# Performance work log

Hardware: AMD Instinct MI355X
Metric: run time of the kernel (lower is better)

Reference implementation:

```python
import jax, jax.numpy as jnp
import numpy as np

C = 684      # encoder out_channels
H = 256      # hidden_size
I = 256      # input_size (embedding dim)
A = 512      # attention dim
V = 415      # word_num (vocab)
CCOV = 256   # coverage conv channels
K = 11       # coverage conv kernel
HF, WF = 32, 128  # feature map H', W'
RATIO = 16
T = 64       # fixed number of decode steps


def gru_cell(x, h, Wih, Whh, bih, bhh):
    # torch.nn.GRUCell semantics
    gi = x @ Wih.T + bih
    gh = h @ Whh.T + bhh
    ir, iz, inn = jnp.split(gi, 3, axis=-1)
    hr, hz, hn = jnp.split(gh, 3, axis=-1)
    r = jax.nn.sigmoid(ir + hr)
    z = jax.nn.sigmoid(iz + hz)
    n = jnp.tanh(inn + r * hn)
    return (1.0 - z) * n + z * h


def setup_inputs() -> dict:
    key = jax.random.key(0)
    ks = list(jax.random.split(key, 40))
    s = 0.05
    def rn(shape):
        return jax.random.normal(ks.pop(), shape, dtype=jnp.float32) * s
    p = {}
    p['cnn_features'] = jax.random.normal(ks.pop(), (1, C, HF, WF), dtype=jnp.float32)
    p['images_mask'] = jnp.ones((1, 1, HF * RATIO, WF * RATIO), dtype=jnp.float32)
    p['emb_table'] = rn((V, I))
    p['W_init'] = rn((H, C)); p['b_init'] = jnp.zeros((H,), jnp.float32)
    p['Wih_in'] = rn((3 * H, I)); p['Whh_in'] = rn((3 * H, H))
    p['bih_in'] = jnp.zeros((3 * H,), jnp.float32); p['bhh_in'] = jnp.zeros((3 * H,), jnp.float32)
    p['Wih_out'] = rn((3 * H, C)); p['Whh_out'] = rn((3 * H, H))
    p['bih_out'] = jnp.zeros((3 * H,), jnp.float32); p['bhh_out'] = jnp.zeros((3 * H,), jnp.float32)
    p['Wq'] = rn((A, H)); p['bq'] = jnp.zeros((A,), jnp.float32)
    p['Wproj'] = rn((A, C)); p['bproj'] = jnp.zeros((A,), jnp.float32)
    p['conv_k'] = rn((CCOV, 1, K, K))
    p['Wcov'] = rn((A, CCOV))
    p['wa'] = rn((A,)); p['ba'] = jnp.zeros((), jnp.float32)
    p['Ws'] = rn((H // 2, H)); p['bs'] = jnp.zeros((H // 2,), jnp.float32)
    p['We'] = rn((H // 2, I)); p['be'] = jnp.zeros((H // 2,), jnp.float32)
    p['Wc'] = rn((H // 2, C)); p['bc'] = jnp.zeros((H // 2,), jnp.float32)
    p['Wv'] = rn((V, H // 2)); p['bv'] = jnp.zeros((V,), jnp.float32)
    return p


def _decode(cnn_features, images_mask, emb_table, W_init, b_init,
            Wih_in, Whh_in, bih_in, bhh_in, Wih_out, Whh_out, bih_out, bhh_out,
            Wq, bq, Wproj, bproj, conv_k, Wcov, wa, ba,
            Ws, bs, We, be, Wc, bc, Wv, bv):
    mask = images_mask[:, :, ::RATIO, ::RATIO]          # [1,1,HF,WF]
    avg = jnp.sum(cnn_features * mask, axis=(2, 3)) / jnp.sum(mask, axis=(2, 3))  # [1,C]
    h0 = jnp.tanh(avg @ W_init.T + b_init)               # init_hidden
    cnn_trans = jnp.einsum('bchw,ac->bhwa', cnn_features, Wproj) + bproj  # 1x1 proj, [1,HF,WF,A]
    mask2d = mask[:, 0] > 0                              # [1,HF,WF]
    emb0 = emb_table[jnp.ones((1,), dtype=jnp.int32)]    # embedding(torch.ones(1).long())
    alpha_sum0 = jnp.zeros((1, 1, HF, WF), dtype=cnn_features.dtype)

    def attend(hidden, alpha_sum):
        q = hidden @ Wq.T + bq                           # [1,A]
        cov = jax.lax.conv_general_dilated(alpha_sum, conv_k, (1, 1), [(K // 2, K // 2)] * 2)
        cov_t = jnp.einsum('bchw,ac->bhwa', cov, Wcov)   # [1,HF,WF,A]
        e = jnp.tanh(q[:, None, None, :] + cov_t + cnn_trans)
        energy = jnp.einsum('bhwa,a->bhw', e, wa) + ba
        energy = jnp.where(mask2d, energy, -1e9)
        alpha = jax.nn.softmax(energy.reshape(1, -1), axis=-1).reshape(energy.shape)
        alpha_sum = alpha_sum + alpha[:, None]
        ctx = jnp.einsum('bhw,bchw->bc', alpha, cnn_features)  # [1,C]
        return ctx, alpha_sum

    def step(carry, _):
        emb, h_par, a_sum = carry
        h1 = gru_cell(emb, h_par, Wih_in, Whh_in, bih_in, bhh_in)      # word_input_gru
        ctx, a_sum = attend(h1, a_sum)                                  # word_attention
        h = gru_cell(ctx, h1, Wih_out, Whh_out, bih_out, bhh_out)       # word_out_gru
        state = (h @ Ws.T + bs) + (emb @ We.T + be) + (ctx @ Wc.T + bc) # fused out state
        prob = state @ Wv.T + bv                                        # word_convert, [1,V]
        word = jnp.argmax(prob, axis=-1)                                # greedy feedback
        emb_next = emb_table[word]
        return (emb_next, h, a_sum), prob[0]

    _, probs = jax.lax.scan(step, (emb0, h0, alpha_sum0), None, length=T)
    return probs  # [T, V]


def reference(cnn_features, images_mask, emb_table, W_init, b_init,
              Wih_in, Whh_in, bih_in, bhh_in, Wih_out, Whh_out, bih_out, bhh_out,
              Wq, bq, Wproj, bproj, conv_k, Wcov, wa, ba,
              Ws, bs, We, be, Wc, bc, Wv, bv):
    return _decode(cnn_features, images_mask, emb_table, W_init, b_init,
                   Wih_in, Whh_in, bih_in, bhh_in, Wih_out, Whh_out, bih_out, bhh_out,
                   Wq, bq, Wproj, bproj, conv_k, Wcov, wa, ba,
                   Ws, bs, We, be, Wc, bc, Wv, bv)
```

## Files before the change

kernel.cpp:

```cpp
#include <hip/hip_runtime.h>
#include <math.h>

#define HF 32
#define WF 128
#define HW 4096
#define C_DIM 684
#define H_DIM 256
#define A_DIM 512
#define V_DIM 415
#define PADR 42
#define PADC 144
#define T_STEPS 64

#define NERG 128
#define CTX0 128
#define NCTXB 86
#define MONO 214
#define RED0 215
#define TAIL0 223
#define HEAT0 239
#define NGRID 255

constexpr int CT_OFF      = 0;
constexpr int KMT_OFF     = CT_OFF + HW * A_DIM;
constexpr int APAD_OFF    = KMT_OFF + 61952;
constexpr int MASK_OFF    = APAD_OFF + 6048;
constexpr int PART_OFF    = MASK_OFF + 4096;
constexpr int AVG_OFF     = PART_OFF + 16384;
constexpr int H0_OFF      = AVG_OFF + 704;
constexpr int QV_OFF      = H0_OFF + 256;
constexpr int H1V_OFF     = QV_OFF + 512;
constexpr int GHOV_OFF    = H1V_OFF + 512;
constexpr int GHNV_OFF    = GHOV_OFF + 1536;
constexpr int GS_OFF      = GHNV_OFF + 768;
constexpr int GPS_OFF     = GS_OFF + 6144;
constexpr int MSUM_OFF    = GPS_OFF + 1024;
constexpr int FLAGS_OFF   = MSUM_OFF + 16;
constexpr int AFR_OFF     = FLAGS_OFF + 4096;
constexpr int AF2R_OFF    = AFR_OFF + 128;
constexpr int H1F_OFF     = AF2R_OFF + 128;
constexpr int DONE_OFF    = H1F_OFF + 128;
constexpr int GFR_OFF     = DONE_OFF + 128;
constexpr int TQR_OFF     = GFR_OFF + 1024;
constexpr int SYNC_END    = TQR_OFF + 2048;
constexpr int PGIO2_OFF   = SYNC_END;
constexpr int PSC2_OFF    = PGIO2_OFF + NCTXB * 768;
constexpr int GI_OFF      = PSC2_OFF + NCTXB * 128;
constexpr int SE_OFF      = GI_OFF + V_DIM * 768;
constexpr int WIHTOUT_OFF = SE_OFF + V_DIM * 128;
constexpr int WCT_OFF     = WIHTOUT_OFF + 684 * 768;
constexpr int WST_OFF     = WCT_OFF + 684 * 128;
constexpr int WVT_OFF     = WST_OFF + 256 * 128;
constexpr int WS_END      = WVT_OFF + 128 * V_DIM;

__device__ __forceinline__ float sigmoidf_(float x) { return 1.f / (1.f + expf(-x)); }
__device__ __forceinline__ float ftanh(float x) {
  float e = __expf(2.f * x);
  return 1.f - 2.f / (e + 1.f);
}

__device__ __forceinline__ float gld(const float* p) {
  int v = __hip_atomic_load((const int*)p, __ATOMIC_RELAXED, __HIP_MEMORY_SCOPE_AGENT);
  return __int_as_float(v);
}
__device__ __forceinline__ void gst(float* p, float x) {
  __hip_atomic_store((int*)p, __float_as_int(x), __ATOMIC_RELAXED, __HIP_MEMORY_SCOPE_AGENT);
}
__device__ __forceinline__ void pollf(int* p, int ph) {
  int it = 0;
  while (__hip_atomic_load(p, __ATOMIC_RELAXED, __HIP_MEMORY_SCOPE_AGENT) < ph) {
    if (it < 4) __builtin_amdgcn_s_sleep(1);
    else if (it < 16) __builtin_amdgcn_s_sleep(4);
    else __builtin_amdgcn_s_sleep(8);
    ++it;
  }
  asm volatile("" ::: "memory");
}
__device__ __forceinline__ void rel_store(int* p, int v) {
  __hip_atomic_store(p, v, __ATOMIC_RELEASE, __HIP_MEMORY_SCOPE_AGENT);
}


__global__ void k_init(const float* __restrict__ imask, float* ws) {
  __shared__ float red[4];
  int tid = threadIdx.x;
  float s = 0.f;
  for (int i = tid; i < HW; i += 256) {
    int h = i >> 7, w = i & 127;
    float m = imask[h * 16 * 2048 + w * 16];
    ws[MASK_OFF + i] = m;
    s += m;
  }
  for (int i = tid; i < PADR * PADC; i += 256) ws[APAD_OFF + i] = 0.f;
  int* sync = (int*)(ws + FLAGS_OFF);
  for (int i = tid; i < 7680; i += 256) sync[i] = 0;
#pragma unroll
  for (int off = 32; off; off >>= 1) s += __shfl_xor(s, off, 64);
  if ((tid & 63) == 0) red[tid >> 6] = s;
  __syncthreads();
  if (tid == 0) ws[MSUM_OFF] = red[0] + red[1] + red[2] + red[3];
}

__global__ void k_avg(const float* __restrict__ cnn, float* ws) {
  __shared__ float red[4];
  int c = blockIdx.x, tid = threadIdx.x;
  const float* row = cnn + c * HW;
  float s = 0.f;
  for (int i = tid; i < HW; i += 256) s += ws[MASK_OFF + i] * row[i];
#pragma unroll
  for (int off = 32; off; off >>= 1) s += __shfl_xor(s, off, 64);
  if ((tid & 63) == 0) red[tid >> 6] = s;
  __syncthreads();
  if (tid == 0) ws[AVG_OFF + c] = (red[0] + red[1] + red[2] + red[3]) / ws[MSUM_OFF];
}

__global__ void k_h0(const float* __restrict__ W_init, const float* __restrict__ b_init, float* ws) {
  __shared__ float a_s[C_DIM];
  int tid = threadIdx.x;
  for (int i = tid; i < C_DIM; i += 256) a_s[i] = ws[AVG_OFF + i];
  __syncthreads();
  const float* wr = W_init + tid * C_DIM;
  float s = b_init[tid];
  for (int k = 0; k < C_DIM; k++) s += a_s[k] * wr[k];
  ws[H0_OFF + tid] = tanhf(s);
}

__global__ __launch_bounds__(512) void k_km(const float* __restrict__ convk,
                                            const float* __restrict__ Wcov, float* ws) {
  __shared__ float kt[256];
  int t = blockIdx.x, a = threadIdx.x;
  if (a < 256) kt[a] = convk[a * 121 + t];
  __syncthreads();
  const float* wr = Wcov + a * 256;
  float s = 0.f;
  for (int c = 0; c < 256; c++) s += kt[c] * wr[c];
  ws[KMT_OFF + a * 121 + t] = s;
}

__global__ void k_ct(const float* __restrict__ cnn, const float* __restrict__ Wproj,
                     const float* __restrict__ bproj, float* ws) {
  __shared__ float As[8][128];
  __shared__ float Bs[8][64];
  int hw0 = blockIdx.x * 128;
  int a0 = blockIdx.y * 64;
  int tid = threadIdx.x;
  int tx = tid & 15, ty = tid >> 4;
  float acc[8][4];
#pragma unroll
  for (int i = 0; i < 8; i++)
#pragma unroll
    for (int j = 0; j < 4; j++) acc[i][j] = 0.f;
  for (int c0 = 0; c0 < C_DIM; c0 += 8) {
    {
      int kk = tid >> 5;
      int m4 = (tid & 31) * 4;
      int c = c0 + kk;
      float4 v = make_float4(0.f, 0.f, 0.f, 0.f);
      if (c < C_DIM) v = *(const float4*)(cnn + c * HW + hw0 + m4);
      *(float4*)&As[kk][m4] = v;
    }
    {
      int n = tid & 63;
      int kk0 = (tid >> 6) * 2;
      const float* wr = Wproj + (a0 + n) * C_DIM + c0;
      Bs[kk0][n]     = (c0 + kk0 < C_DIM) ? wr[kk0] : 0.f;
      Bs[kk0 + 1][n] = (c0 + kk0 + 1 < C_DIM) ? wr[kk0 + 1] : 0.f;
    }
    __syncthreads();
#pragma unroll
    for (int kk = 0; kk < 8; kk++) {
      float a8[8], b4[4];
#pragma unroll
      for (int i = 0; i < 8; i++) a8[i] = As[kk][ty * 8 + i];
#pragma unroll
      for (int j = 0; j < 4; j++) b4[j] = Bs[kk][tx * 4 + j];
#pragma unroll
      for (int i = 0; i < 8; i++)
#pragma unroll
        for (int j = 0; j < 4; j++) acc[i][j] += a8[i] * b4[j];
    }
    __syncthreads();
  }
#pragma unroll
  for (int i = 0; i < 8; i++) {
    int hw = hw0 + ty * 8 + i;
#pragma unroll
    for (int j = 0; j < 4; j++) {
      int a = a0 + tx * 4 + j;
      ws[CT_OFF + hw * A_DIM + a] = acc[i][j] + bproj[a];
    }
  }
}

__global__ void k_gi(const float* __restrict__ emb_table, const float* __restrict__ Wih_in,
                     const float* __restrict__ bih_in, float* ws) {
  __shared__ float e_s[256];
  int v = blockIdx.x, tid = threadIdx.x;
  e_s[tid] = emb_table[v * 256 + tid];
  __syncthreads();
#pragma unroll
  for (int r = 0; r < 3; r++) {
    int m = r * 256 + tid;
    const float* wr = Wih_in + m * 256;
    float s = bih_in[m];
    for (int k = 0; k < 256; k++) s += e_s[k] * wr[k];
    ws[GI_OFF + v * 768 + m] = s;
  }
}

__global__ void k_se(const float* __restrict__ emb_table, const float* __restrict__ We,
                     const float* __restrict__ be, float* ws) {
  __shared__ float e_s[256];
  int v = blockIdx.x, tid = threadIdx.x;
  e_s[tid] = emb_table[v * 256 + tid];
  e_s[tid + 128] = emb_table[v * 256 + tid + 128];
  __syncthreads();
  const float* wr = We + tid * 256;
  float s = be[tid];
  for (int k = 0; k < 256; k++) s += e_s[k] * wr[k];
  ws[SE_OFF + v * 128 + tid] = s;
}

__global__ void k_tr(const float* __restrict__ in, float* __restrict__ out, int M, int Kd) {
  int total = M * Kd;
  for (int i = blockIdx.x * blockDim.x + threadIdx.x; i < total; i += gridDim.x * blockDim.x) {
    int m = i / Kd, k = i - m * Kd;
    out[k * M + m] = in[i];
  }
}

__global__ __launch_bounds__(512) void k_pre0(const float* __restrict__ Whh_in,
                                              const float* __restrict__ bhh_in, float* ws) {
  __shared__ float h0s[256];
  __shared__ float ghn48[48];
  const int s = blockIdx.x, tid = threadIdx.x;
  const int j0 = s * 16;
  if (tid < 256) h0s[tid] = ws[H0_OFF + tid];
  __syncthreads();
  {
    int r = tid >> 3, l = tid & 7;
    if (r < 48) {
      int mg = (r >> 4) * 256 + j0 + (r & 15);
      const float* wr = Whh_in + mg * 256 + l * 32;
      float sm = 0.f;
#pragma unroll
      for (int k = 0; k < 32; k++) sm += h0s[l * 32 + k] * wr[k];
#pragma unroll
      for (int off = 4; off; off >>= 1) sm += __shfl_xor(sm, off, 8);
      if (l == 0) ghn48[r] = sm + bhh_in[mg];
    }
  }
  __syncthreads();
  if (tid < 16) {
    int j = j0 + tid;
    const float* gi = ws + GI_OFF + 1 * 768;
    float r = sigmoidf_(gi[j] + ghn48[tid]);
    float z = sigmoidf_(gi[256 + j] + ghn48[16 + tid]);
    float n = tanhf(gi[512 + j] + r * ghn48[32 + tid]);
    gst(ws + H1V_OFF + j, (1.f - z) * n + z * h0s[j]);
  }
}

__global__ __launch_bounds__(512) void k_pre1(const float* __restrict__ Wq,
                                              const float* __restrict__ Whh_out,
                                              const float* __restrict__ bhh_out, float* ws) {
  __shared__ float h1s[256];
  const int s = blockIdx.x, tid = threadIdx.x;
  if (tid < 256) h1s[tid] = gld(ws + H1V_OFF + tid);
  __syncthreads();
  {
    int ap = tid >> 4, l = tid & 15;
    int a = s * 32 + ap;
    const float* wr = Wq + a * 256 + l * 16;
    float sm = 0.f;
#pragma unroll
    for (int k = 0; k < 16; k++) sm += h1s[l * 16 + k] * wr[k];
#pragma unroll
    for (int off = 8; off; off >>= 1) sm += __shfl_xor(sm, off, 16);
    if (l == 0) gst(ws + QV_OFF + a, sm);
  }
  {
    int r = tid >> 3, l = tid & 7;
    if (r < 48) {
      int m = s * 48 + r;
      const float* wr = Whh_out + m * 256 + l * 32;
      float sm = 0.f;
#pragma unroll
      for (int k = 0; k < 32; k++) sm += h1s[l * 32 + k] * wr[k];
#pragma unroll
      for (int off = 4; off; off >>= 1) sm += __shfl_xor(sm, off, 8);
      if (l == 0) gst(ws + GHOV_OFF + m, sm + bhh_out[m]);
    }
  }
}

__global__ void k_go(float* ws) {
  int tid = threadIdx.x;
  if (tid < 128) ((int*)(ws + TQR_OFF))[tid * 16] = 1;
}


__global__ __launch_bounds__(512) void k_steps(
    const float* __restrict__ cnn, const float* __restrict__ Whh_in,
    const float* __restrict__ Whh_out, const float* __restrict__ Wq,
    const float* __restrict__ bq, const float* __restrict__ wa, const float* __restrict__ ba,
    const float* __restrict__ bih_out, const float* __restrict__ bhh_out,
    const float* __restrict__ bhh_in,
    const float* __restrict__ bs_, const float* __restrict__ bc_, const float* __restrict__ bv_,
    float* ws, float* __restrict__ out) {
  __shared__ __align__(16) float S[40016];

  const int bid = blockIdx.x, tid = threadIdx.x;
  int* flags = (int*)(ws + FLAGS_OFF);
  int* afr   = (int*)(ws + AFR_OFF);
  int* af2r  = (int*)(ws + AF2R_OFF);
  int* h1f   = (int*)(ws + H1F_OFF);
  int* donef = (int*)(ws + DONE_OFF);
  int* gfr   = (int*)(ws + GFR_OFF);
  int* tqr   = (int*)(ws + TQR_OFF);

  if (bid < NERG) {
    const int h_row = bid >> 2, aq = bid & 3, a0 = aq * 128;
    const int al = tid & 127, hslot = tid >> 7;
    float* km    = S;
    float* ct    = S + 16896;
    float* patch = S + 33280;
    float* maskv = S + 34864;
    float* redE  = S + 34992;
    for (int i = tid; i < 128 * 132; i += 512) {
      int a = i / 132, j = i - a * 132;
      int dy = j / 12, dx = j - dy * 12;
      km[i] = (dx < 11) ? ws[KMT_OFF + (a0 + a) * 121 + dy * 11 + dx] : 0.f;
    }
    for (int i = tid; i < 128 * 128; i += 512) {
      int w = i >> 7, aa = i & 127;
      ct[i] = ws[CT_OFF + (h_row * 128 + w) * 512 + a0 + aa];
    }
    if (tid < 128) maskv[tid] = ws[MASK_OFF + h_row * 128 + tid];
    const float bq_a = bq[a0 + al], wa_a = wa[a0 + al], ba0 = ba[0];
    __syncthreads();

#pragma unroll 1
    for (int t = 0; t < T_STEPS; t++) {
      if (tid == 0) pollf(&af2r[(bid & 7) * 16], t);
      __syncthreads();
      for (int i = tid; i < 11 * 138; i += 512) {
        int r = i / 138, c = i - r * 138;
        patch[r * 144 + c] = gld(ws + APAD_OFF + (h_row + r) * PADC + c);
      }
      __syncthreads();
      float acc[2][16];
#pragma unroll
      for (int p = 0; p < 2; p++)
#pragma unroll
        for (int i = 0; i < 16; i++) acc[p][i] = 0.f;
      const int wbase0 = hslot * 32;
#pragma unroll 1
      for (int dy = 0; dy < 11; dy++) {
        float kv[12];
        {
          const float* kb = &km[al * 132 + dy * 12];
          *(float4*)&kv[0] = *(const float4*)&kb[0];
          *(float4*)&kv[4] = *(const float4*)&kb[4];
          *(float4*)&kv[8] = *(const float4*)&kb[8];
        }
#pragma unroll
        for (int p = 0; p < 2; p++) {
          float row[28];
          const float* pr = &patch[dy * 144 + wbase0 + p * 16];
#pragma unroll
          for (int i = 0; i < 7; i++) *(float4*)&row[i * 4] = *(const float4*)&pr[i * 4];
#pragma unroll
          for (int dx = 0; dx < 11; dx++)
#pragma unroll
            for (int wi = 0; wi < 16; wi++) acc[p][wi] += kv[dx] * row[wi + dx];
        }
      }
      if (tid < 16) pollf(&tqr[(tid * 8 + (bid & 7)) * 16], t + 1);
      __syncthreads();
      float qa = bq_a + gld(ws + QV_OFF + a0 + al);
#pragma unroll 1
      for (int p = 0; p < 2; p++) {
        const int wbase = wbase0 + p * 16;
#pragma unroll
        for (int wi = 0; wi < 16; wi++) {
          float x = acc[p][wi] + qa + ct[(wbase + wi) * 128 + al];
          float v = ftanh(x) * wa_a;
#pragma unroll
          for (int off = 32; off; off >>= 1) v += __shfl_xor(v, off, 64);
          if ((tid & 63) == 0) redE[(tid >> 6) * 16 + wi] = v;
        }
        __syncthreads();
        if (tid < 64) {
          int hs2 = tid >> 4, wi = tid & 15;
          int w = hs2 * 32 + p * 16 + wi;
          float e = redE[(hs2 * 2) * 16 + wi] + redE[(hs2 * 2 + 1) * 16 + wi];
          float val = (maskv[w] > 0.f) ? (e + (aq == 0 ? ba0 : 0.f)) : -2.5e8f;
          gst(ws + PART_OFF + aq * 4096 + h_row * 128 + w, val);
        }
        __syncthreads();
      }
      if (tid == 0) rel_store(&flags[bid * 16], t + 1);
    }

  } else if (bid < CTX0 + NCTXB) {
    const int cb = bid - CTX0, c0 = cb * 8;
    float* cnnS = S;
    float* wio  = S + 32768;
    float* wct  = S + 38912;
    float* redC = S + 39936;
    float* ctxv = S + 40000;
    float* invp = S + 40008;
    for (int i = tid; i < 8 * 4096; i += 512) {
      int c = c0 + (i >> 12);
      cnnS[i] = (c < C_DIM) ? cnn[c * 4096 + (i & 4095)] : 0.f;
    }
    for (int i = tid; i < 8 * 768; i += 512) {
      int c = c0 + i / 768;
      wio[i] = (c < C_DIM) ? ws[WIHTOUT_OFF + c * 768 + (i % 768)] : 0.f;
    }
    for (int i = tid; i < 8 * 128; i += 512) {
      int c = c0 + (i >> 7);
      wct[i] = (c < C_DIM) ? ws[WCT_OFF + c * 128 + (i & 127)] : 0.f;
    }
    __syncthreads();

#pragma unroll 1
    for (int t = 0; t < T_STEPS; t++) {
      if (tid == 0) pollf(&afr[(bid & 7) * 16], t + 1);
      __syncthreads();
      float ev[8];
      float ssum = 0.f;
#pragma unroll
      for (int j = 0; j < 8; j++) {
        int hw = j * 512 + tid;
        float e = gld(ws + PART_OFF + hw) + gld(ws + PART_OFF + 4096 + hw) +
                  gld(ws + PART_OFF + 8192 + hw) + gld(ws + PART_OFF + 12288 + hw);
        ev[j] = __expf(e);
        ssum += ev[j];
      }
#pragma unroll
      for (int off = 32; off; off >>= 1) ssum += __shfl_xor(ssum, off, 64);
      if ((tid & 63) == 0) redC[tid >> 6] = ssum;
      __syncthreads();
      if (tid == 0) {
        float s2 = 0.f;
#pragma unroll
        for (int i = 0; i < 8; i++) s2 += redC[i];
        invp[0] = 1.f / s2;
      }
      __syncthreads();
      float inv = invp[0];
      if (cb < 8) {
        int hw = cb * 512 + tid;
        int hh = hw >> 7, ww = hw & 127;
        float* ap = ws + APAD_OFF + (hh + 5) * PADC + ww + 5;
        gst(ap, gld(ap) + ev[cb] * inv);
      }
#pragma unroll
      for (int cc = 0; cc < 8; cc++) {
        float p = 0.f;
#pragma unroll
        for (int j = 0; j < 8; j++) p += ev[j] * cnnS[cc * 4096 + j * 512 + tid];
#pragma unroll
        for (int off = 32; off; off >>= 1) p += __shfl_xor(p, off, 64);
        if ((tid & 63) == 0) redC[(tid >> 6) * 8 + cc] = p;
      }
      __syncthreads();
      if (tid < 8) {
        float cv = 0.f;
#pragma unroll
        for (int w2 = 0; w2 < 8; w2++) cv += redC[w2 * 8 + tid];
        ctxv[tid] = cv * inv;
      }
      __syncthreads();
      for (int m = tid; m < 768; m += 512) {
        float s2 = 0.f;
#pragma unroll
        for (int cc = 0; cc < 8; cc++) s2 += ctxv[cc] * wio[cc * 768 + m];
        gst(ws + PGIO2_OFF + cb * 768 + m, s2);
      }
      if (tid < 128) {
        float s2 = 0.f;
#pragma unroll
        for (int cc = 0; cc < 8; cc++) s2 += ctxv[cc] * wct[cc * 128 + tid];
        gst(ws + PSC2_OFF + cb * 128 + tid, s2);
      }
      __syncthreads();
      if (tid == 0) rel_store(&flags[(CTX0 + cb) * 16], t + 1);
    }

  } else if (bid == MONO) {
    float* wst  = S;
    float* mh   = S + 32768;
    float* mst  = S + 33024;
    float* sval = S + 33152;
    int*   sidx = (int*)(S + 33664);
    int*   mwp  = (int*)(S + 34176);
    int*   mwn  = (int*)(S + 34177);
    for (int i = tid; i < 256 * 128; i += 512) wst[i] = ws[WST_OFF + i];
    if (tid == 0) mwp[0] = 1;
    __syncthreads();

#pragma unroll 1
    for (int t = 0; t < T_STEPS; t++) {
      const int par = t & 1;
      if (tid < 128) pollf(&flags[tid * 16], t + 1);
      __syncthreads();
      if (tid < 8) rel_store(&afr[tid * 16], t + 1);
      if (tid < 8) pollf(&gfr[(tid * 8 + 7) * 16], t + 1);
      __syncthreads();
      if (tid < 256) {
        float g0 = bih_out[tid], g1 = bih_out[256 + tid], g2 = bih_out[512 + tid];
#pragma unroll
        for (int j = 0; j < 8; j++) {
          const float* gs = ws + GS_OFF + j * 768;
          g0 += gld(gs + tid);
          g1 += gld(gs + 256 + tid);
          g2 += gld(gs + 512 + tid);
        }
        const float* gh = ws + GHOV_OFF + par * 768;
        float o0 = gld(gh + tid), o1 = gld(gh + 256 + tid), o2 = gld(gh + 512 + tid);
        float h1v = gld(ws + H1V_OFF + par * 256 + tid);
        float r = sigmoidf_(g0 + o0);
        float z = sigmoidf_(g1 + o1);
        float n = tanhf(g2 + r * o2);
        mh[tid] = (1.f - z) * n + z * h1v;
      }
      __syncthreads();
      if (tid < 128) {
        float s = bs_[tid] + bc_[tid] + ws[SE_OFF + mwp[0] * 128 + tid];
#pragma unroll
        for (int j = 0; j < 8; j++) s += gld(ws + GPS_OFF + j * 128 + tid);
        const float* wt = wst + tid;
#pragma unroll 8
        for (int k = 0; k < 256; k++) s += mh[k] * wt[k * 128];
        mst[tid] = s;
      }
      __syncthreads();
      {
        float best = -3.4e38f;
        if (tid < V_DIM) {
          float p2 = bv_[tid];
          const float* wt = ws + WVT_OFF + tid;
#pragma unroll 8
          for (int k = 0; k < 128; k++) p2 += mst[k] * wt[k * V_DIM];
          out[t * V_DIM + tid] = p2;
          best = p2;
        }
        sval[tid] = best;
        sidx[tid] = tid;
        __syncthreads();
        for (int m = 256; m >= 1; m >>= 1) {
          if (tid < m) {
            float ov = sval[tid + m];
            int oi = sidx[tid + m];
            if (ov > sval[tid] || (ov == sval[tid] && oi < sidx[tid])) {
              sval[tid] = ov;
              sidx[tid] = oi;
            }
          }
          __syncthreads();
        }
        if (tid == 0) mwn[0] = sidx[0];
        __syncthreads();
      }
      if (tid < 16) pollf(&flags[(224 + tid) * 16], t + 1);
      __syncthreads();
      if (tid < 256) {
        const float* gi = ws + GI_OFF + mwn[0] * 768;
        float n0 = gld(ws + GHNV_OFF + tid);
        float n1 = gld(ws + GHNV_OFF + 256 + tid);
        float n2 = gld(ws + GHNV_OFF + 512 + tid);
        float r = sigmoidf_(gi[tid] + n0);
        float z = sigmoidf_(gi[256 + tid] + n1);
        float n = tanhf(gi[512 + tid] + r * n2);
        gst(ws + H1V_OFF + ((t + 1) & 1) * 256 + tid, (1.f - z) * n + z * mh[tid]);
      }
      __syncthreads();
      if (tid < 8) rel_store(&h1f[tid * 16], t + 1);
      if (tid == 0) mwp[0] = mwn[0];
      __syncthreads();
    }
    if (tid < 8) rel_store(&donef[tid * 16], 1);

  } else if (bid < TAIL0) {
    const int j = bid - RED0;
    const int lo = j * 11, hi = (j == 7) ? 86 : (lo + 11);
#pragma unroll 1
    for (int t = 0; t < T_STEPS; t++) {
      if (tid < hi - lo) pollf(&flags[(CTX0 + lo + tid) * 16], t + 1);
      __syncthreads();
      if (j == 0 && tid < 8) rel_store(&af2r[tid * 16], t + 1);
      for (int m = tid; m < 768; m += 512) {
        float s = 0.f;
        for (int cb = lo; cb < hi; cb++) s += gld(ws + PGIO2_OFF + cb * 768 + m);
        gst(ws + GS_OFF + j * 768 + m, s);
      }
      if (tid < 128) {
        float s = 0.f;
        for (int cb = lo; cb < hi; cb++) s += gld(ws + PSC2_OFF + cb * 128 + tid);
        gst(ws + GPS_OFF + j * 128 + tid, s);
      }
      __syncthreads();
      if (tid < 8) rel_store(&gfr[(j * 8 + tid) * 16], t + 1);
    }

  } else if (bid < HEAT0) {
    const int s = bid - TAIL0;
    float* whinS = S;
    float* whoS  = S + 12288;
    float* wqS   = S + 24576;
    float* hS    = S + 32768;
    float* h1S   = S + 33024;
    for (int i = tid; i < 12288; i += 512) whinS[i] = Whh_in[s * 12288 + i];
    for (int i = tid; i < 12288; i += 512) whoS[i] = Whh_out[s * 12288 + i];
    for (int i = tid; i < 8192; i += 512) wqS[i] = Wq[s * 8192 + i];
    __syncthreads();

#pragma unroll 1
    for (int t = 0; t < T_STEPS; t++) {
      const int par = t & 1;
      if (tid < 8) pollf(&gfr[(tid * 8 + (s & 7)) * 16], t + 1);
      __syncthreads();
      if (tid < 256) {
        float g0 = bih_out[tid], g1 = bih_out[256 + tid], g2 = bih_out[512 + tid];
#pragma unroll
        for (int j = 0; j < 8; j++) {
          const float* gs = ws + GS_OFF + j * 768;
          g0 += gld(gs + tid);
          g1 += gld(gs + 256 + tid);
          g2 += gld(gs + 512 + tid);
        }
        const float* gh = ws + GHOV_OFF + par * 768;
        float o0 = gld(gh + tid), o1 = gld(gh + 256 + tid), o2 = gld(gh + 512 + tid);
        float h1v = gld(ws + H1V_OFF + par * 256 + tid);
        float r = sigmoidf_(g0 + o0);
        float z = sigmoidf_(g1 + o1);
        float n = tanhf(g2 + r * o2);
        hS[tid] = (1.f - z) * n + z * h1v;
      }
      __syncthreads();
      {
        int r = tid >> 3, l = tid & 7;
        if (r < 48) {
          int m = s * 48 + r;
          const float* wr = &whinS[r * 256 + l * 32];
          const float* hb = &hS[l * 32];
          float sm = 0.f;
#pragma unroll
          for (int k = 0; k < 32; k += 4) {
            float4 w4 = *(const float4*)&wr[k];
            float4 h4 = *(const float4*)&hb[k];
            sm += w4.x * h4.x + w4.y * h4.y + w4.z * h4.z + w4.w * h4.w;
          }
#pragma unroll
          for (int off = 4; off; off >>= 1) sm += __shfl_xor(sm, off, 8);
          if (l == 0) gst(ws + GHNV_OFF + m, sm + bhh_in[m]);
        }
      }
      __syncthreads();
      if (tid == 0) rel_store(&flags[(224 + s) * 16], t + 1);
      if (tid == 0) pollf(&h1f[(s & 7) * 16], t + 1);
      __syncthreads();
      if (tid < 256) h1S[tid] = gld(ws + H1V_OFF + ((t + 1) & 1) * 256 + tid);
      __syncthreads();
      {
        int r = tid >> 3, l = tid & 7;
        if (r < 48) {
          int m = s * 48 + r;
          const float* wr = &whoS[r * 256 + l * 32];
          const float* hb = &h1S[l * 32];
          float sm = 0.f;
#pragma unroll
          for (int k = 0; k < 32; k += 4) {
            float4 w4 = *(const float4*)&wr[k];
            float4 h4 = *(const float4*)&hb[k];
            sm += w4.x * h4.x + w4.y * h4.y + w4.z * h4.z + w4.w * h4.w;
          }
#pragma unroll
          for (int off = 4; off; off >>= 1) sm += __shfl_xor(sm, off, 8);
          if (l == 0) gst(ws + GHOV_OFF + ((t + 1) & 1) * 768 + m, sm + bhh_out[m]);
        }
      }
      {
        int ap = tid >> 4, l = tid & 15;
        int a = s * 32 + ap;
        const float* wr = &wqS[ap * 256 + l * 16];
        const float* hb = &h1S[l * 16];
        float sm = 0.f;
#pragma unroll
        for (int k = 0; k < 16; k++) sm += wr[k] * hb[k];
#pragma unroll
        for (int off = 8; off; off >>= 1) sm += __shfl_xor(sm, off, 16);
        if (l == 0) gst(ws + QV_OFF + a, sm);
      }
      __syncthreads();
      if (tid < 8) rel_store(&tqr[(s * 8 + tid) * 16], t + 2);
    }

  } else {
    volatile int* hstop = (volatile int*)(S + 100);
    if (tid == 0) *hstop = 0;
    __syncthreads();
    if (tid < 256) {
      float a0 = 1.f + (float)tid, a1 = 2.f, a2 = 3.f, a3 = 4.f;
      const float b = 0.9999f, c = 1e-7f;
      while (*hstop == 0) {
#pragma unroll
        for (int i = 0; i < 16; i++) {
          a0 = __builtin_fmaf(a0, b, c);
          a1 = __builtin_fmaf(a1, b, c);
          a2 = __builtin_fmaf(a2, b, c);
          a3 = __builtin_fmaf(a3, b, c);
        }
        if (tid == 0 &&
            __hip_atomic_load(&donef[(bid & 7) * 16], __ATOMIC_RELAXED,
                              __HIP_MEMORY_SCOPE_AGENT) != 0)
          *hstop = 1;
      }
      asm volatile("" :: "v"(a0), "v"(a1), "v"(a2), "v"(a3));
    }
  }
}


extern "C" void kernel_launch(void* const* d_in, const int* in_sizes, int n_in,
                              void* d_out, int out_size, void* d_ws, size_t ws_size,
                              hipStream_t stream) {
  (void)in_sizes; (void)n_in; (void)out_size; (void)ws_size;
  const float* cnn      = (const float*)d_in[0];
  const float* imask    = (const float*)d_in[1];
  const float* emb_tab  = (const float*)d_in[2];
  const float* W_init   = (const float*)d_in[3];
  const float* b_init   = (const float*)d_in[4];
  const float* Wih_in   = (const float*)d_in[5];
  const float* Whh_in   = (const float*)d_in[6];
  const float* bih_in   = (const float*)d_in[7];
  const float* bhh_in   = (const float*)d_in[8];
  const float* Wih_out  = (const float*)d_in[9];
  const float* Whh_out  = (const float*)d_in[10];
  const float* bih_out  = (const float*)d_in[11];
  const float* bhh_out  = (const float*)d_in[12];
  const float* Wq       = (const float*)d_in[13];
  const float* bq       = (const float*)d_in[14];
  const float* Wproj    = (const float*)d_in[15];
  const float* bproj    = (const float*)d_in[16];
  const float* convk    = (const float*)d_in[17];
  const float* Wcov     = (const float*)d_in[18];
  const float* wa       = (const float*)d_in[19];
  const float* ba       = (const float*)d_in[20];
  const float* Ws_      = (const float*)d_in[21];
  const float* bs_      = (const float*)d_in[22];
  const float* We_      = (const float*)d_in[23];
  const float* be_      = (const float*)d_in[24];
  const float* Wc_      = (const float*)d_in[25];
  const float* bc_      = (const float*)d_in[26];
  const float* Wv_      = (const float*)d_in[27];
  const float* bv_      = (const float*)d_in[28];
  float* ws  = (float*)d_ws;
  float* out = (float*)d_out;

  k_init<<<1, 256, 0, stream>>>(imask, ws);
  k_avg<<<C_DIM, 256, 0, stream>>>(cnn, ws);
  k_h0<<<1, 256, 0, stream>>>(W_init, b_init, ws);
  k_km<<<121, 512, 0, stream>>>(convk, Wcov, ws);
  k_ct<<<dim3(HW / 128, A_DIM / 64), 256, 0, stream>>>(cnn, Wproj, bproj, ws);
  k_gi<<<V_DIM, 256, 0, stream>>>(emb_tab, Wih_in, bih_in, ws);
  k_se<<<V_DIM, 128, 0, stream>>>(emb_tab, We_, be_, ws);
  k_tr<<<512, 256, 0, stream>>>(Wih_out, ws + WIHTOUT_OFF, 768, 684);
  k_tr<<<512, 256, 0, stream>>>(Wc_, ws + WCT_OFF, 128, 684);
  k_tr<<<512, 256, 0, stream>>>(Ws_, ws + WST_OFF, 128, 256);
  k_tr<<<512, 256, 0, stream>>>(Wv_, ws + WVT_OFF, 415, 128);
  k_pre0<<<16, 512, 0, stream>>>(Whh_in, bhh_in, ws);
  k_pre1<<<16, 512, 0, stream>>>(Wq, Whh_out, bhh_out, ws);
  k_go<<<1, 256, 0, stream>>>(ws);

  k_steps<<<NGRID, 512, 0, stream>>>(cnn, Whh_in, Whh_out, Wq, bq, wa, ba,
                                     bih_out, bhh_out, bhh_in, bs_, bc_, bv_, ws, out);
}
```

Baseline: 2.980 ms.

## Move context projection into reducer blocks and pad LDS weight rows

```diff
diff --git a/kernel.cpp b/kernel.cpp
--- a/kernel.cpp
+++ b/kernel.cpp
@@ -34,7 +34,8 @@
 constexpr int GHNV_OFF    = GHOV_OFF + 1536;
 constexpr int GS_OFF      = GHNV_OFF + 768;
 constexpr int GPS_OFF     = GS_OFF + 6144;
-constexpr int MSUM_OFF    = GPS_OFF + 1024;
+constexpr int CTXV_OFF    = GPS_OFF + 1024;
+constexpr int MSUM_OFF    = CTXV_OFF + 704;
 constexpr int FLAGS_OFF   = MSUM_OFF + 16;
 constexpr int AFR_OFF     = FLAGS_OFF + 4096;
 constexpr int AF2R_OFF    = AFR_OFF + 128;
@@ -43,9 +44,7 @@
 constexpr int GFR_OFF     = DONE_OFF + 128;
 constexpr int TQR_OFF     = GFR_OFF + 1024;
 constexpr int SYNC_END    = TQR_OFF + 2048;
-constexpr int PGIO2_OFF   = SYNC_END;
-constexpr int PSC2_OFF    = PGIO2_OFF + NCTXB * 768;
-constexpr int GI_OFF      = PSC2_OFF + NCTXB * 128;
+constexpr int GI_OFF      = SYNC_END;
 constexpr int SE_OFF      = GI_OFF + V_DIM * 768;
 constexpr int WIHTOUT_OFF = SE_OFF + V_DIM * 128;
 constexpr int WCT_OFF     = WIHTOUT_OFF + 684 * 768;
@@ -406,22 +405,12 @@
   } else if (bid < CTX0 + NCTXB) {
     const int cb = bid - CTX0, c0 = cb * 8;
     float* cnnS = S;
-    float* wio  = S + 32768;
-    float* wct  = S + 38912;
-    float* redC = S + 39936;
-    float* ctxv = S + 40000;
-    float* invp = S + 40008;
+    float* redC = S + 32768;
+    float* ctxv = S + 32832;
+    float* invp = S + 32840;
     for (int i = tid; i < 8 * 4096; i += 512) {
       int c = c0 + (i >> 12);
       cnnS[i] = (c < C_DIM) ? cnn[c * 4096 + (i & 4095)] : 0.f;
-    }
-    for (int i = tid; i < 8 * 768; i += 512) {
-      int c = c0 + i / 768;
-      wio[i] = (c < C_DIM) ? ws[WIHTOUT_OFF + c * 768 + (i % 768)] : 0.f;
-    }
-    for (int i = tid; i < 8 * 128; i += 512) {
-      int c = c0 + (i >> 7);
-      wct[i] = (c < C_DIM) ? ws[WCT_OFF + c * 128 + (i & 127)] : 0.f;
     }
     __syncthreads();
 
@@ -471,20 +460,7 @@
         float cv = 0.f;
 #pragma unroll
         for (int w2 = 0; w2 < 8; w2++) cv += redC[w2 * 8 + tid];
-        ctxv[tid] = cv * inv;
-      }
-      __syncthreads();
-      for (int m = tid; m < 768; m += 512) {
-        float s2 = 0.f;
-#pragma unroll
-        for (int cc = 0; cc < 8; cc++) s2 += ctxv[cc] * wio[cc * 768 + m];
-        gst(ws + PGIO2_OFF + cb * 768 + m, s2);
-      }
-      if (tid < 128) {
-        float s2 = 0.f;
-#pragma unroll
-        for (int cc = 0; cc < 8; cc++) s2 += ctxv[cc] * wct[cc * 128 + tid];
-        gst(ws + PSC2_OFF + cb * 128 + tid, s2);
+        gst(ws + CTXV_OFF + c0 + tid, cv * inv);
       }
       __syncthreads();
       if (tid == 0) rel_store(&flags[(CTX0 + cb) * 16], t + 1);
@@ -587,19 +563,23 @@
   } else if (bid < TAIL0) {
     const int j = bid - RED0;
     const int lo = j * 11, hi = (j == 7) ? 86 : (lo + 11);
+    const int c0 = lo * 8, c1 = (hi * 8 < C_DIM) ? hi * 8 : C_DIM;
+    float* cvS = S;
 #pragma unroll 1
     for (int t = 0; t < T_STEPS; t++) {
       if (tid < hi - lo) pollf(&flags[(CTX0 + lo + tid) * 16], t + 1);
       __syncthreads();
       if (j == 0 && tid < 8) rel_store(&af2r[tid * 16], t + 1);
+      if (tid < c1 - c0) cvS[tid] = gld(ws + CTXV_OFF + c0 + tid);
+      __syncthreads();
       for (int m = tid; m < 768; m += 512) {
         float s = 0.f;
-        for (int cb = lo; cb < hi; cb++) s += gld(ws + PGIO2_OFF + cb * 768 + m);
+        for (int c = c0; c < c1; c++) s += cvS[c - c0] * ws[WIHTOUT_OFF + c * 768 + m];
         gst(ws + GS_OFF + j * 768 + m, s);
       }
       if (tid < 128) {
         float s = 0.f;
-        for (int cb = lo; cb < hi; cb++) s += gld(ws + PSC2_OFF + cb * 128 + tid);
+        for (int c = c0; c < c1; c++) s += cvS[c - c0] * ws[WCT_OFF + c * 128 + tid];
         gst(ws + GPS_OFF + j * 128 + tid, s);
       }
       __syncthreads();
@@ -609,13 +589,13 @@
   } else if (bid < HEAT0) {
     const int s = bid - TAIL0;
     float* whinS = S;
-    float* whoS  = S + 12288;
-    float* wqS   = S + 24576;
-    float* hS    = S + 32768;
-    float* h1S   = S + 33024;
-    for (int i = tid; i < 12288; i += 512) whinS[i] = Whh_in[s * 12288 + i];
-    for (int i = tid; i < 12288; i += 512) whoS[i] = Whh_out[s * 12288 + i];
-    for (int i = tid; i < 8192; i += 512) wqS[i] = Wq[s * 8192 + i];
+    float* whoS  = S + 12672;
+    float* wqS   = S + 25344;
+    float* hS    = S + 33792;
+    float* h1S   = S + 34048;
+    for (int i = tid; i < 48 * 256; i += 512) whinS[(i >> 8) * 264 + (i & 255)] = Whh_in[s * 12288 + i];
+    for (int i = tid; i < 48 * 256; i += 512) whoS[(i >> 8) * 264 + (i & 255)] = Whh_out[s * 12288 + i];
+    for (int i = tid; i < 32 * 256; i += 512) wqS[(i >> 8) * 264 + (i & 255)] = Wq[s * 8192 + i];
     __syncthreads();
 
 #pragma unroll 1
@@ -645,13 +625,11 @@
         int r = tid >> 3, l = tid & 7;
         if (r < 48) {
           int m = s * 48 + r;
-          const float* wr = &whinS[r * 256 + l * 32];
-          const float* hb = &hS[l * 32];
           float sm = 0.f;
 #pragma unroll
-          for (int k = 0; k < 32; k += 4) {
-            float4 w4 = *(const float4*)&wr[k];
-            float4 h4 = *(const float4*)&hb[k];
+          for (int jj = 0; jj < 8; jj++) {
+            float4 w4 = *(const float4*)&whinS[r * 264 + jj * 32 + l * 4];
+            float4 h4 = *(const float4*)&hS[jj * 32 + l * 4];
             sm += w4.x * h4.x + w4.y * h4.y + w4.z * h4.z + w4.w * h4.w;
           }
 #pragma unroll
@@ -669,13 +647,11 @@
         int r = tid >> 3, l = tid & 7;
         if (r < 48) {
           int m = s * 48 + r;
-          const float* wr = &whoS[r * 256 + l * 32];
-          const float* hb = &h1S[l * 32];
           float sm = 0.f;
 #pragma unroll
-          for (int k = 0; k < 32; k += 4) {
-            float4 w4 = *(const float4*)&wr[k];
-            float4 h4 = *(const float4*)&hb[k];
+          for (int jj = 0; jj < 8; jj++) {
+            float4 w4 = *(const float4*)&whoS[r * 264 + jj * 32 + l * 4];
+            float4 h4 = *(const float4*)&h1S[jj * 32 + l * 4];
             sm += w4.x * h4.x + w4.y * h4.y + w4.z * h4.z + w4.w * h4.w;
           }
 #pragma unroll
@@ -686,11 +662,13 @@
       {
         int ap = tid >> 4, l = tid & 15;
         int a = s * 32 + ap;
-        const float* wr = &wqS[ap * 256 + l * 16];
-        const float* hb = &h1S[l * 16];
         float sm = 0.f;
 #pragma unroll
-        for (int k = 0; k < 16; k++) sm += wr[k] * hb[k];
+        for (int jj = 0; jj < 4; jj++) {
+          float4 w4 = *(const float4*)&wqS[ap * 264 + jj * 64 + l * 4];
+          float4 h4 = *(const float4*)&h1S[jj * 64 + l * 4];
+          sm += w4.x * h4.x + w4.y * h4.y + w4.z * h4.z + w4.w * h4.w;
+        }
 #pragma unroll
         for (int off = 8; off; off >>= 1) sm += __shfl_xor(sm, off, 16);
         if (l == 0) gst(ws + QV_OFF + a, sm);
```

Result: slower. 4.075 ms (+36.8%).
